# Kernel optimization log

Measured on AMD Instinct MI355X. Metric: run time of the kernel, lower is better.

## Reference

```python
import jax, jax.numpy as jnp
import numpy as np

N_CLASSES = 256
N_AUDIO_CHANS = 1
N_CHANS = 128
N_RES = 128
N_SKIP = 256
N_END = 256
KERNEL = 2
N_LAYERS = 10
N_STACKS = 3
DILATIONS = [2 ** i for _ in range(N_STACKS) for i in range(N_LAYERS)]
L = len(DILATIONS)
DN = ('NCW', 'OIW', 'NCW')


def setup_inputs() -> dict:
    key = jax.random.key(0)
    ks = jax.random.split(key, 16)
    s = 0.05  # small init keeps 30-layer residual stack numerically tame
    inp = {
        'x': jax.random.normal(ks[0], (4, N_AUDIO_CHANS, 16384), jnp.float32),
        'w_shift': jax.random.normal(ks[1], (N_CHANS, N_AUDIO_CHANS, KERNEL), jnp.float32) * s,
        'b_shift': jnp.zeros((N_CHANS,), jnp.float32),
        'conv_w': jax.random.normal(ks[2], (L, 2 * N_RES, N_CHANS, KERNEL), jnp.float32) * s,
        'conv_b': jnp.zeros((L, 2 * N_RES), jnp.float32),
        'res_w': jax.random.normal(ks[3], (L, N_CHANS, N_RES), jnp.float32) * s,
        'res_b': jnp.zeros((L, N_CHANS), jnp.float32),
        'skip_w': jax.random.normal(ks[4], (L, N_SKIP, N_RES), jnp.float32) * s,
        'skip_b': jnp.zeros((L, N_SKIP), jnp.float32),
        'a_w': jax.random.normal(ks[5], (N_END, N_SKIP), jnp.float32) * s,
        'a_b': jnp.zeros((N_END,), jnp.float32),
        'b_w': jax.random.normal(ks[6], (N_CLASSES * N_AUDIO_CHANS, N_END), jnp.float32) * s,
        'b_b': jnp.zeros((N_CLASSES * N_AUDIO_CHANS,), jnp.float32),
    }
    return inp


def _causal_conv(x, w, b, dilation):
    # left-pad by (k-1)*dilation so outputs depend only on past/present
    pad = (w.shape[-1] - 1) * dilation
    xp = jnp.pad(x, ((0, 0), (0, 0), (pad, 0)))
    y = jax.lax.conv_general_dilated(xp, w, window_strides=(1,), padding='VALID',
                                     rhs_dilation=(dilation,), dimension_numbers=DN)
    return y + b[None, :, None]


def reference(x, w_shift, b_shift, conv_w, conv_b, res_w, res_b,
              skip_w, skip_b, a_w, a_b, b_w, b_b):
    N, C, W = x.shape
    # shifted conv: shift input right by one (prepend 0, drop last), then causal conv
    xs = jnp.pad(x, ((0, 0), (0, 0), (1, 0)))[:, :, :-1]
    h = _causal_conv(xs, w_shift, b_shift, 1)  # (N, n_chans, W)

    skips = jnp.zeros((N, N_SKIP, W), h.dtype)
    for l in range(L):
        g = _causal_conv(h, conv_w[l], conv_b[l], DILATIONS[l])  # (N, 2*res, W)
        a, b_gate = jnp.split(g, 2, axis=1)
        gated = a * jax.nn.sigmoid(b_gate)                        # GLU, (N, res, W)
        h = jnp.einsum('or,nrw->now', res_w[l], gated) + res_b[l][None, :, None] + h
        skips = skips + jnp.einsum('or,nrw->now', skip_w[l], gated) + skip_b[l][None, :, None]

    z = jax.nn.relu(skips)
    z = jax.nn.relu(jnp.einsum('os,nsw->now', a_w, z) + a_b[None, :, None])
    logits = jnp.einsum('oe,new->now', b_w, z) + b_b[None, :, None]
    return logits.reshape(N, N_CLASSES, N_AUDIO_CHANS, W)
```

## Files before the change

### kernel.cpp

```cpp
#include <hip/hip_runtime.h>
#include <math.h>


#define NB 4
#define WLEN 16384
#define C 128
#define S 256
#define NLAYERS 30
#define TT 64
#define NTB (WLEN / TT)
#define XROW 264
#define GROW 136

#define SX(row, c) ((row) * 128 + ((c) ^ (((row) & 7) << 3)))

typedef _Float16 half8 __attribute__((ext_vector_type(8)));
typedef _Float16 half4 __attribute__((ext_vector_type(4)));
typedef float floatx4 __attribute__((ext_vector_type(4)));

__device__ __forceinline__ float sigmoidf_(float v) {
    return 1.0f / (1.0f + __expf(-v));
}

__global__ void prep_kernel(const float* __restrict__ conv_w,
                            const float* __restrict__ res_w,
                            const float* __restrict__ skip_w,
                            const float* __restrict__ a_w,
                            const float* __restrict__ b_w,
                            const float* __restrict__ conv_b,
                            const float* __restrict__ skip_b,
                            _Float16* __restrict__ cw,
                            _Float16* __restrict__ rsw,
                            _Float16* __restrict__ skw,
                            _Float16* __restrict__ aw,
                            _Float16* __restrict__ bw,
                            float* __restrict__ cbp,
                            float* __restrict__ ssum) {
    const int ncw = NLAYERS * 256 * 256;
    const int nrs = NLAYERS * 128 * 128;
    const int nsk = NLAYERS * 256 * 128;
    const int nab = 256 * 256;
    const int ncb = NLAYERS * 256;
    const int total = ncw + nrs + nsk + nab + nab + ncb + 256;
    for (int idx = blockIdx.x * blockDim.x + threadIdx.x; idx < total;
         idx += gridDim.x * blockDim.x) {
        int i = idx;
        if (i < ncw) {
            int j = i & 7, lane = (i >> 3) & 63, rest = i >> 9;
            int ks = rest & 7; rest >>= 3;
            int mt = rest & 15; int l = rest >> 4;
            int mp = mt * 16 + (lane & 15);
            int orow = (mp >> 1) + (mp & 1) * 128;
            int k = ks * 32 + (lane >> 4) * 8 + j;
            int tap = k >> 7, c = k & 127;
            cw[i] = (_Float16)conv_w[(((size_t)l * 256 + orow) * 128 + c) * 2 + tap];
        } else if (i < ncw + nrs) {
            i -= ncw;
            int j = i & 7, lane = (i >> 3) & 63, rest = i >> 9;
            int ks = rest & 3; rest >>= 2;
            int mt = rest & 7; int l = rest >> 3;
            int m = mt * 16 + (lane & 15);
            int k = ks * 32 + (lane >> 4) * 8 + j;
            rsw[i] = (_Float16)res_w[((size_t)l * 128 + m) * 128 + k];
        } else if (i < ncw + nrs + nsk) {
            i -= ncw + nrs;
            int j = i & 7, lane = (i >> 3) & 63, rest = i >> 9;
            int ks = rest & 3; rest >>= 2;
            int mt = rest & 15; int l = rest >> 4;
            int m = mt * 16 + (lane & 15);
            int k = ks * 32 + (lane >> 4) * 8 + j;
            skw[i] = (_Float16)skip_w[((size_t)l * 256 + m) * 128 + k];
        } else if (i < ncw + nrs + nsk + nab) {
            i -= ncw + nrs + nsk;
            int j = i & 7, lane = (i >> 3) & 63, rest = i >> 9;
            int ks = rest & 7; int mt = rest >> 3;
            aw[i] = (_Float16)a_w[(mt * 16 + (lane & 15)) * 256 + ks * 32 + (lane >> 4) * 8 + j];
        } else if (i < ncw + nrs + nsk + 2 * nab) {
            i -= ncw + nrs + nsk + nab;
            int j = i & 7, lane = (i >> 3) & 63, rest = i >> 9;
            int ks = rest & 7; int mt = rest >> 3;
            bw[i] = (_Float16)b_w[(mt * 16 + (lane & 15)) * 256 + ks * 32 + (lane >> 4) * 8 + j];
        } else if (i < ncw + nrs + nsk + 2 * nab + ncb) {
            i -= ncw + nrs + nsk + 2 * nab;
            int mp = i & 255; int l = i >> 8;
            cbp[i] = conv_b[l * 256 + (mp >> 1) + (mp & 1) * 128];
        } else {
            i -= ncw + nrs + nsk + 2 * nab + ncb;
            float s = 0.f;
            for (int l = 0; l < NLAYERS; ++l) s += skip_b[l * 256 + i];
            ssum[i] = s;
        }
    }
}

__global__ void front_kernel(const float* __restrict__ x,
                             const float* __restrict__ w_shift,
                             const float* __restrict__ b_shift,
                             _Float16* __restrict__ h) {
    const int n = blockIdx.y;
    const int t = blockIdx.x * 256 + threadIdx.x;
    float x1 = (t >= 1) ? x[n * WLEN + t - 1] : 0.0f;
    float x2 = (t >= 2) ? x[n * WLEN + t - 2] : 0.0f;
    _Float16* hq = h + ((size_t)n * WLEN + t) * 128;
    #pragma unroll
    for (int c0 = 0; c0 < 128; c0 += 8) {
        half8 v;
        #pragma unroll
        for (int j = 0; j < 8; ++j) {
            int c = c0 + j;
            v[j] = (_Float16)fmaf(w_shift[2 * c], x2,
                                  fmaf(w_shift[2 * c + 1], x1, b_shift[c]));
        }
        *(half8*)&hq[c0] = v;
    }
}

template <int E0, int NL, int NT, int HALO, bool FIRST>
__global__ __launch_bounds__(512)
__attribute__((amdgpu_waves_per_eu(2, 4))) void stack_kernel(
    const _Float16* __restrict__ h_in, _Float16* __restrict__ h_out,
    _Float16* __restrict__ chunk,
    const _Float16* __restrict__ cw0, const float* __restrict__ cb0,
    const _Float16* __restrict__ rsw0, const float* __restrict__ rb0,
    const _Float16* __restrict__ skw0, const float* __restrict__ ssum) {
    constexpr int WR = NT * 16;
    __shared__ _Float16 SMEM[2 * WR * 128];
    _Float16* H = SMEM;
    _Float16* G = SMEM + WR * 128;
    const int n = blockIdx.y, tb = blockIdx.x, t0 = tb * TT;
    const int tid = threadIdx.x;
    const int wave = __builtin_amdgcn_readfirstlane(tid >> 6);
    const int lane = tid & 63, q = lane >> 4, ml = lane & 15;

    floatx4 sacc[2][4];
    if (FIRST) {
        #pragma unroll
        for (int mt = 0; mt < 2; ++mt)
            #pragma unroll
            for (int r = 0; r < 4; ++r) {
                float bias = ssum[32 * wave + mt * 16 + q * 4 + r];
                #pragma unroll
                for (int nt = 0; nt < 4; ++nt) sacc[mt][nt][r] = bias;
            }
    } else {
        const _Float16* cp = chunk + ((size_t)n * NTB + tb) * 16384;
        #pragma unroll
        for (int mt = 0; mt < 2; ++mt)
            #pragma unroll
            for (int nt = 0; nt < 4; ++nt) {
                size_t o = (size_t)((((wave * 2 + mt) * 4) + nt) * 64 + lane) * 4;
                half4 v = *(const half4*)&cp[o];
                #pragma unroll
                for (int r = 0; r < 4; ++r) sacc[mt][nt][r] = (float)v[r];
            }
    }

    const _Float16* hn = h_in + (size_t)n * WLEN * 128;
    #pragma unroll
    for (int it = 0; it < (WR * 16 + 511) / 512; ++it) {
        int idx = it * 512 + tid;
        if (idx < WR * 16) {
            int seg = idx & 15;
            int w = idx >> 4;
            int src_t = t0 - HALO + w;
            half8 v = (half8)(_Float16)0.0f;
            if (src_t >= 0)
                v = *(const half8*)&hn[(size_t)src_t * 128 + seg * 8];
            *(half8*)&H[SX(w, seg * 8)] = v;
        }
    }
    __syncthreads();

    const _Float16* cw  = cw0;
    const float*    cb  = cb0;
    const _Float16* rsw = rsw0;
    const float*    rb  = rb0;
    const _Float16* skw = skw0;

    #pragma clang loop unroll(disable)
    for (int j = 0; j < NL; ++j) {
        const int d = 1 << (E0 + j);

        #pragma unroll
        for (int base = 0; base < NT; base += 4) {
            floatx4 acc[2][4];
            #pragma unroll
            for (int mt = 0; mt < 2; ++mt)
                #pragma unroll
                for (int r = 0; r < 4; ++r) {
                    float bias = cb[32 * wave + mt * 16 + q * 4 + r];
                    #pragma unroll
                    for (int nt = 0; nt < 4; ++nt) acc[mt][nt][r] = bias;
                }
            #pragma unroll
            for (int hp = 0; hp < 2; ++hp) {
                for (int ks = 0; ks < 4; ++ks) {
                    half8 a[2];
                    #pragma unroll
                    for (int mt = 0; mt < 2; ++mt)
                        a[mt] = *(const half8*)&cw[((((2 * wave + mt) * 8) + hp * 4 + ks) * 64 + lane) * 8];
                    #pragma unroll
                    for (int nt = 0; nt < 4; ++nt) {
                        if (base + nt < NT) {
                            int row = (base + nt) * 16 + ml;
                            if (!hp) { row -= d; if (row < 0) row = 0; }
                            half8 b = *(const half8*)&H[SX(row, ks * 32 + q * 8)];
                            #pragma unroll
                            for (int mt = 0; mt < 2; ++mt)
                                acc[mt][nt] = __builtin_amdgcn_mfma_f32_16x16x32_f16(a[mt], b, acc[mt][nt], 0, 0, 0);
                        }
                    }
                }
            }
            #pragma unroll
            for (int mt = 0; mt < 2; ++mt)
                #pragma unroll
                for (int nt = 0; nt < 4; ++nt) {
                    if (base + nt < NT) {
                        float g0 = acc[mt][nt][0] * sigmoidf_(acc[mt][nt][1]);
                        float g1 = acc[mt][nt][2] * sigmoidf_(acc[mt][nt][3]);
                        _Float16 p[2] = {(_Float16)g0, (_Float16)g1};
                        *(uint32_t*)&G[SX((base + nt) * 16 + ml, 16 * wave + mt * 8 + 2 * q)] = *(uint32_t*)p;
                    }
                }
        }
        __syncthreads();

        #pragma unroll
        for (int ks = 0; ks < 4; ++ks) {
            half8 a[2];
            #pragma unroll
            for (int mt = 0; mt < 2; ++mt)
                a[mt] = *(const half8*)&skw[((((2 * wave + mt) * 4) + ks) * 64 + lane) * 8];
            #pragma unroll
            for (int nt = 0; nt < 4; ++nt) {
                half8 b = *(const half8*)&G[SX(HALO + nt * 16 + ml, ks * 32 + q * 8)];
                #pragma unroll
                for (int mt = 0; mt < 2; ++mt)
                    sacc[mt][nt] = __builtin_amdgcn_mfma_f32_16x16x32_f16(a[mt], b, sacc[mt][nt], 0, 0, 0);
            }
        }

        #pragma unroll
        for (int base = 0; base < NT; base += 4) {
            floatx4 racc[4];
            #pragma unroll
            for (int r = 0; r < 4; ++r) {
                float bias = rb[16 * wave + q * 4 + r];
                #pragma unroll
                for (int nt = 0; nt < 4; ++nt) racc[nt][r] = bias;
            }
            #pragma unroll
            for (int ks = 0; ks < 4; ++ks) {
                half8 a = *(const half8*)&rsw[(((wave * 4) + ks) * 64 + lane) * 8];
                #pragma unroll
                for (int nt = 0; nt < 4; ++nt) {
                    if (base + nt < NT) {
                        half8 b = *(const half8*)&G[SX((base + nt) * 16 + ml, ks * 32 + q * 8)];
                        racc[nt] = __builtin_amdgcn_mfma_f32_16x16x32_f16(a, b, racc[nt], 0, 0, 0);
                    }
                }
            }
            #pragma unroll
            for (int nt = 0; nt < 4; ++nt) {
                if (base + nt < NT) {
                    int w = (base + nt) * 16 + ml;
                    int c = 16 * wave + q * 4;
                    half4 hv = *(const half4*)&H[SX(w, c)];
                    half4 o;
                    #pragma unroll
                    for (int r = 0; r < 4; ++r)
                        o[r] = (_Float16)(racc[nt][r] + (float)hv[r]);
                    *(half4*)&H[SX(w, c)] = o;
                }
            }
        }
        __syncthreads();

        cw  += 65536; cb += 256; rsw += 16384; rb += 128; skw += 32768;
    }

    _Float16* ho = h_out + (size_t)n * WLEN * 128;
    #pragma unroll
    for (int it = 0; it < 2; ++it) {
        int idx = it * 512 + tid;
        int seg = idx & 15;
        int w64 = idx >> 4;
        *(half8*)&ho[(size_t)(t0 + w64) * 128 + seg * 8] =
            *(const half8*)&H[SX(HALO + w64, seg * 8)];
    }

    {
        _Float16* cp = chunk + ((size_t)n * NTB + tb) * 16384;
        #pragma unroll
        for (int mt = 0; mt < 2; ++mt)
            #pragma unroll
            for (int nt = 0; nt < 4; ++nt) {
                size_t o = (size_t)((((wave * 2 + mt) * 4) + nt) * 64 + lane) * 4;
                half4 v;
                #pragma unroll
                for (int r = 0; r < 4; ++r) v[r] = (_Float16)sacc[mt][nt][r];
                *(half4*)&cp[o] = v;
            }
    }
}

__global__ __launch_bounds__(512, 8) void layer_kernel(
    const _Float16* __restrict__ h_in, _Float16* __restrict__ h_out,
    _Float16* __restrict__ chunk,
    const _Float16* __restrict__ cw, const float* __restrict__ cb,
    const _Float16* __restrict__ rsw, const float* __restrict__ rb,
    const _Float16* __restrict__ skw, int d) {
    __shared__ _Float16 SMEM[2 * TT * GROW];
    _Float16* X0 = SMEM;
    _Float16* X1 = SMEM + TT * GROW;
    _Float16* G  = X0;
    const int n = blockIdx.y, tb = blockIdx.x, t0 = tb * TT;
    const int tid = threadIdx.x;
    const int wave = __builtin_amdgcn_readfirstlane(tid >> 6);
    const int lane = tid & 63, q = lane >> 4, ml = lane & 15;

    const _Float16* hn = h_in + (size_t)n * WLEN * 128;
    #pragma unroll
    for (int it = 0; it < 4; ++it) {
        int idx = it * 512 + tid;
        int seg = idx & 15;
        int rowc = (idx >> 4) & 63;
        int tap = idx >> 10;
        int src_t = t0 + rowc - (tap ? 0 : d);
        half8 v = (half8)(_Float16)0.0f;
        if (src_t >= 0)
            v = *(const half8*)&hn[(size_t)src_t * 128 + seg * 8];
        _Float16* Xb = tap ? X1 : X0;
        *(half8*)&Xb[rowc * GROW + seg * 8] = v;
    }
    __syncthreads();

    floatx4 acc[2][4];
    #pragma unroll
    for (int mt = 0; mt < 2; ++mt)
        #pragma unroll
        for (int r = 0; r < 4; ++r) {
            float bias = cb[32 * wave + mt * 16 + q * 4 + r];
            #pragma unroll
            for (int nt = 0; nt < 4; ++nt) acc[mt][nt][r] = bias;
        }
    #pragma unroll
    for (int hp = 0; hp < 2; ++hp) {
        const _Float16* Xb = hp ? X1 : X0;
        for (int ks = 0; ks < 4; ++ks) {
            half8 a[2];
            #pragma unroll
            for (int mt = 0; mt < 2; ++mt)
                a[mt] = *(const half8*)&cw[((((2 * wave + mt) * 8) + hp * 4 + ks) * 64 + lane) * 8];
            #pragma unroll
            for (int nt = 0; nt < 4; ++nt) {
                half8 b = *(const half8*)&Xb[(nt * 16 + ml) * GROW + ks * 32 + q * 8];
                #pragma unroll
                for (int mt = 0; mt < 2; ++mt)
                    acc[mt][nt] = __builtin_amdgcn_mfma_f32_16x16x32_f16(a[mt], b, acc[mt][nt], 0, 0, 0);
            }
        }
    }
    __syncthreads();

    #pragma unroll
    for (int mt = 0; mt < 2; ++mt)
        #pragma unroll
        for (int nt = 0; nt < 4; ++nt) {
            float g0 = acc[mt][nt][0] * sigmoidf_(acc[mt][nt][1]);
            float g1 = acc[mt][nt][2] * sigmoidf_(acc[mt][nt][3]);
            _Float16 p[2] = {(_Float16)g0, (_Float16)g1};
            *(uint32_t*)&G[(nt * 16 + ml) * GROW + 16 * wave + mt * 8 + 2 * q] = *(uint32_t*)p;
        }
    __syncthreads();

    {
        floatx4 sacc[2][4];
        #pragma unroll
        for (int mt = 0; mt < 2; ++mt)
            #pragma unroll
            for (int nt = 0; nt < 4; ++nt)
                #pragma unroll
                for (int r = 0; r < 4; ++r) sacc[mt][nt][r] = 0.0f;
        #pragma unroll
        for (int ks = 0; ks < 4; ++ks) {
            half8 a[2];
            #pragma unroll
            for (int mt = 0; mt < 2; ++mt)
                a[mt] = *(const half8*)&skw[((((2 * wave + mt) * 4) + ks) * 64 + lane) * 8];
            #pragma unroll
            for (int nt = 0; nt < 4; ++nt) {
                half8 b = *(const half8*)&G[(nt * 16 + ml) * GROW + ks * 32 + q * 8];
                #pragma unroll
                for (int mt = 0; mt < 2; ++mt)
                    sacc[mt][nt] = __builtin_amdgcn_mfma_f32_16x16x32_f16(a[mt], b, sacc[mt][nt], 0, 0, 0);
            }
        }
        _Float16* cp = chunk + ((size_t)n * NTB + tb) * 16384;
        #pragma unroll
        for (int mt = 0; mt < 2; ++mt)
            #pragma unroll
            for (int nt = 0; nt < 4; ++nt) {
                size_t o = (size_t)((((wave * 2 + mt) * 4) + nt) * 64 + lane) * 4;
                half4 v = *(const half4*)&cp[o];
                half4 w;
                #pragma unroll
                for (int r = 0; r < 4; ++r)
                    w[r] = (_Float16)(sacc[mt][nt][r] + (float)v[r]);
                *(half4*)&cp[o] = w;
            }
    }

    {
        floatx4 racc[4];
        #pragma unroll
        for (int r = 0; r < 4; ++r) {
            float bias = rb[16 * wave + q * 4 + r];
            #pragma unroll
            for (int nt = 0; nt < 4; ++nt) racc[nt][r] = bias;
        }
        #pragma unroll
        for (int ks = 0; ks < 4; ++ks) {
            half8 a = *(const half8*)&rsw[(((wave * 4) + ks) * 64 + lane) * 8];
            #pragma unroll
            for (int nt = 0; nt < 4; ++nt) {
                half8 b = *(const half8*)&G[(nt * 16 + ml) * GROW + ks * 32 + q * 8];
                racc[nt] = __builtin_amdgcn_mfma_f32_16x16x32_f16(a, b, racc[nt], 0, 0, 0);
            }
        }
        _Float16* ho = h_out + (size_t)n * WLEN * 128;
        #pragma unroll
        for (int nt = 0; nt < 4; ++nt) {
            int tt = nt * 16 + ml;
            int c = 16 * wave + q * 4;
            half4 hv = *(const half4*)&X1[tt * GROW + c];
            half4 o;
            #pragma unroll
            for (int r = 0; r < 4; ++r)
                o[r] = (_Float16)(racc[nt][r] + (float)hv[r]);
            *(half4*)&ho[(size_t)(t0 + tt) * 128 + c] = o;
        }
    }
}

__global__ __launch_bounds__(512, 8) void last_head_kernel(
    const _Float16* __restrict__ h_in, const _Float16* __restrict__ chunk,
    float* __restrict__ out,
    const _Float16* __restrict__ cw, const float* __restrict__ cb,
    const _Float16* __restrict__ skw,
    const _Float16* __restrict__ aw, const float* __restrict__ ab,
    const _Float16* __restrict__ bw, const float* __restrict__ bb, int d) {
    __shared__ _Float16 SMEM[2 * TT * GROW];
    _Float16* X0 = SMEM;
    _Float16* X1 = SMEM + TT * GROW;
    _Float16* G  = X0;
    _Float16* X  = SMEM;
    const int n = blockIdx.y, tb = blockIdx.x, t0 = tb * TT;
    const int tid = threadIdx.x;
    const int wave = __builtin_amdgcn_readfirstlane(tid >> 6);
    const int lane = tid & 63, q = lane >> 4, ml = lane & 15;

    const _Float16* hn = h_in + (size_t)n * WLEN * 128;
    #pragma unroll
    for (int it = 0; it < 4; ++it) {
        int idx = it * 512 + tid;
        int seg = idx & 15;
        int rowc = (idx >> 4) & 63;
        int tap = idx >> 10;
        int src_t = t0 + rowc - (tap ? 0 : d);
        half8 v = (half8)(_Float16)0.0f;
        if (src_t >= 0)
            v = *(const half8*)&hn[(size_t)src_t * 128 + seg * 8];
        _Float16* Xb = tap ? X1 : X0;
        *(half8*)&Xb[rowc * GROW + seg * 8] = v;
    }
    __syncthreads();

    floatx4 acc[2][4];
    #pragma unroll
    for (int mt = 0; mt < 2; ++mt)
        #pragma unroll
        for (int r = 0; r < 4; ++r) {
            float bias = cb[32 * wave + mt * 16 + q * 4 + r];
            #pragma unroll
            for (int nt = 0; nt < 4; ++nt) acc[mt][nt][r] = bias;
        }
    #pragma unroll
    for (int hp = 0; hp < 2; ++hp) {
        const _Float16* Xb = hp ? X1 : X0;
        for (int ks = 0; ks < 4; ++ks) {
            half8 a[2];
            #pragma unroll
            for (int mt = 0; mt < 2; ++mt)
                a[mt] = *(const half8*)&cw[((((2 * wave + mt) * 8) + hp * 4 + ks) * 64 + lane) * 8];
            #pragma unroll
            for (int nt = 0; nt < 4; ++nt) {
                half8 b = *(const half8*)&Xb[(nt * 16 + ml) * GROW + ks * 32 + q * 8];
                #pragma unroll
                for (int mt = 0; mt < 2; ++mt)
                    acc[mt][nt] = __builtin_amdgcn_mfma_f32_16x16x32_f16(a[mt], b, acc[mt][nt], 0, 0, 0);
            }
        }
    }
    __syncthreads();

    #pragma unroll
    for (int mt = 0; mt < 2; ++mt)
        #pragma unroll
        for (int nt = 0; nt < 4; ++nt) {
            float g0 = acc[mt][nt][0] * sigmoidf_(acc[mt][nt][1]);
            float g1 = acc[mt][nt][2] * sigmoidf_(acc[mt][nt][3]);
            _Float16 p[2] = {(_Float16)g0, (_Float16)g1};
            *(uint32_t*)&G[(nt * 16 + ml) * GROW + 16 * wave + mt * 8 + 2 * q] = *(uint32_t*)p;
        }
    __syncthreads();

    half4 z[2][4];
    {
        floatx4 sacc[2][4];
        #pragma unroll
        for (int mt = 0; mt < 2; ++mt)
            #pragma unroll
            for (int nt = 0; nt < 4; ++nt)
                #pragma unroll
                for (int r = 0; r < 4; ++r) sacc[mt][nt][r] = 0.0f;
        #pragma unroll
        for (int ks = 0; ks < 4; ++ks) {
            half8 a[2];
            #pragma unroll
            for (int mt = 0; mt < 2; ++mt)
                a[mt] = *(const half8*)&skw[((((2 * wave + mt) * 4) + ks) * 64 + lane) * 8];
            #pragma unroll
            for (int nt = 0; nt < 4; ++nt) {
                half8 b = *(const half8*)&G[(nt * 16 + ml) * GROW + ks * 32 + q * 8];
                #pragma unroll
                for (int mt = 0; mt < 2; ++mt)
                    sacc[mt][nt] = __builtin_amdgcn_mfma_f32_16x16x32_f16(a[mt], b, sacc[mt][nt], 0, 0, 0);
            }
        }
        const _Float16* cp = chunk + ((size_t)n * NTB + tb) * 16384;
        #pragma unroll
        for (int mt = 0; mt < 2; ++mt)
            #pragma unroll
            for (int nt = 0; nt < 4; ++nt) {
                size_t o = (size_t)((((wave * 2 + mt) * 4) + nt) * 64 + lane) * 4;
                half4 v = *(const half4*)&cp[o];
                #pragma unroll
                for (int r = 0; r < 4; ++r) {
                    _Float16 s = (_Float16)(sacc[mt][nt][r] + (float)v[r]);
                    z[mt][nt][r] = (_Float16)fmaxf((float)s, 0.0f);
                }
            }
    }
    __syncthreads();

    #pragma unroll
    for (int mt = 0; mt < 2; ++mt)
        #pragma unroll
        for (int nt = 0; nt < 4; ++nt)
            *(half4*)&X[(nt * 16 + ml) * XROW + 32 * wave + mt * 16 + q * 4] = z[mt][nt];
    __syncthreads();

    #pragma unroll
    for (int mt = 0; mt < 2; ++mt)
        #pragma unroll
        for (int r = 0; r < 4; ++r) {
            float bias = ab[32 * wave + mt * 16 + q * 4 + r];
            #pragma unroll
            for (int nt = 0; nt < 4; ++nt) acc[mt][nt][r] = bias;
        }
    for (int ks = 0; ks < 8; ++ks) {
        half8 a[2];
        #pragma unroll
        for (int mt = 0; mt < 2; ++mt)
            a[mt] = *(const half8*)&aw[((((2 * wave + mt) * 8) + ks) * 64 + lane) * 8];
        #pragma unroll
        for (int nt = 0; nt < 4; ++nt) {
            half8 b = *(const half8*)&X[(nt * 16 + ml) * XROW + ks * 32 + q * 8];
            #pragma unroll
            for (int mt = 0; mt < 2; ++mt)
                acc[mt][nt] = __builtin_amdgcn_mfma_f32_16x16x32_f16(a[mt], b, acc[mt][nt], 0, 0, 0);
        }
    }
    __syncthreads();
    #pragma unroll
    for (int mt = 0; mt < 2; ++mt)
        #pragma unroll
        for (int nt = 0; nt < 4; ++nt) {
            half4 zz;
            #pragma unroll
            for (int r = 0; r < 4; ++r)
                zz[r] = (_Float16)fmaxf(acc[mt][nt][r], 0.0f);
            *(half4*)&X[(nt * 16 + ml) * XROW + 32 * wave + mt * 16 + q * 4] = zz;
        }
    __syncthreads();

    #pragma unroll
    for (int mt = 0; mt < 2; ++mt)
        #pragma unroll
        for (int r = 0; r < 4; ++r) {
            float bias = bb[32 * wave + mt * 16 + q * 4 + r];
            #pragma unroll
            for (int nt = 0; nt < 4; ++nt) acc[mt][nt][r] = bias;
        }
    for (int ks = 0; ks < 8; ++ks) {
        half8 a[2];
        #pragma unroll
        for (int mt = 0; mt < 2; ++mt)
            a[mt] = *(const half8*)&bw[((((2 * wave + mt) * 8) + ks) * 64 + lane) * 8];
        #pragma unroll
        for (int nt = 0; nt < 4; ++nt) {
            half8 b = *(const half8*)&X[(nt * 16 + ml) * XROW + ks * 32 + q * 8];
            #pragma unroll
            for (int mt = 0; mt < 2; ++mt)
                acc[mt][nt] = __builtin_amdgcn_mfma_f32_16x16x32_f16(a[mt], b, acc[mt][nt], 0, 0, 0);
        }
    }
    float* on = out + (size_t)n * S * WLEN;
    #pragma unroll
    for (int mt = 0; mt < 2; ++mt)
        #pragma unroll
        for (int nt = 0; nt < 4; ++nt)
            #pragma unroll
            for (int r = 0; r < 4; ++r) {
                int o = 32 * wave + mt * 16 + q * 4 + r;
                int tt = t0 + nt * 16 + ml;
                on[(size_t)o * WLEN + tt] = acc[mt][nt][r];
            }
}

extern "C" void kernel_launch(void* const* d_in, const int* in_sizes, int n_in,
                              void* d_out, int out_size, void* d_ws, size_t ws_size,
                              hipStream_t stream) {
    (void)in_sizes; (void)n_in; (void)out_size; (void)ws_size;
    const float* x       = (const float*)d_in[0];
    const float* w_shift = (const float*)d_in[1];
    const float* b_shift = (const float*)d_in[2];
    const float* conv_w  = (const float*)d_in[3];
    const float* conv_b  = (const float*)d_in[4];
    const float* res_w   = (const float*)d_in[5];
    const float* res_b   = (const float*)d_in[6];
    const float* skip_w  = (const float*)d_in[7];
    const float* skip_b  = (const float*)d_in[8];
    const float* a_w     = (const float*)d_in[9];
    const float* a_b     = (const float*)d_in[10];
    const float* b_w     = (const float*)d_in[11];
    const float* b_b     = (const float*)d_in[12];
    float* out = (float*)d_out;

    char* ws = (char*)d_ws;
    size_t off = 0;
    _Float16* hA    = (_Float16*)(ws + off); off += (size_t)NB * WLEN * 128 * 2;
    _Float16* hB    = (_Float16*)(ws + off); off += (size_t)NB * WLEN * 128 * 2;
    _Float16* chunk = (_Float16*)(ws + off); off += (size_t)NB * NTB * 16384 * 2;
    _Float16* cw  = (_Float16*)(ws + off); off += (size_t)NLAYERS * 256 * 256 * 2;
    _Float16* rsw = (_Float16*)(ws + off); off += (size_t)NLAYERS * 128 * 128 * 2;
    _Float16* skw = (_Float16*)(ws + off); off += (size_t)NLAYERS * 256 * 128 * 2;
    _Float16* aw  = (_Float16*)(ws + off); off += 256 * 256 * 2;
    _Float16* bw  = (_Float16*)(ws + off); off += 256 * 256 * 2;
    float* cbp  = (float*)(ws + off); off += (size_t)NLAYERS * 256 * 4;
    float* ssum = (float*)(ws + off); off += 256 * 4;

    prep_kernel<<<512, 256, 0, stream>>>(conv_w, res_w, skip_w, a_w, b_w,
                                         conv_b, skip_b,
                                         cw, rsw, skw, aw, bw, cbp, ssum);
    front_kernel<<<dim3(WLEN / 256, NB), 256, 0, stream>>>(x, w_shift, b_shift, hA);

    const dim3 grid(NTB, NB);
    _Float16* hin = hA;
    _Float16* hout = hB;
    for (int s = 0; s < 3; ++s) {
        const int l0 = s * 10;
        if (s == 0)
            stack_kernel<0, 4, 5, 16, true><<<grid, 512, 0, stream>>>(
                hin, hout, chunk,
                cw + (size_t)l0 * 65536, cbp + l0 * 256,
                rsw + (size_t)l0 * 16384, res_b + l0 * 128,
                skw + (size_t)l0 * 32768, ssum);
        else
            stack_kernel<0, 4, 5, 16, false><<<grid, 512, 0, stream>>>(
                hin, hout, chunk,
                cw + (size_t)l0 * 65536, cbp + l0 * 256,
                rsw + (size_t)l0 * 16384, res_b + l0 * 128,
                skw + (size_t)l0 * 32768, ssum);
        { _Float16* tmp = hin; hin = hout; hout = tmp; }
        for (int jj = 4; jj < 10; ++jj) {
            const int l = l0 + jj;
            const int dil = 1 << jj;
            if (l == NLAYERS - 1) {
                last_head_kernel<<<grid, 512, 0, stream>>>(
                    hin, chunk, out,
                    cw + (size_t)l * 65536, cbp + l * 256,
                    skw + (size_t)l * 32768,
                    aw, a_b, bw, b_b, dil);
            } else {
                layer_kernel<<<grid, 512, 0, stream>>>(
                    hin, hout, chunk,
                    cw + (size_t)l * 65536, cbp + l * 256,
                    rsw + (size_t)l * 16384, res_b + l * 128,
                    skw + (size_t)l * 32768, dil);
                _Float16* tmp = hin; hin = hout; hout = tmp;
            }
        }
    }
}
```

Baseline: 1.026 ms.

## Zero-pad activation buffers and load layer inputs directly into LDS

Activation buffers get a zeroed left-padding region of 512 time rows per batch, so causal loads no longer need bounds checks. The layer kernels now fetch input tiles with global_load_lds, writing straight to shared memory without passing through registers. Shared-memory tiles switch from padded rows to the XOR-swizzled layout to avoid bank conflicts, and the global source address is pre-swizzled to match. This adds an extra pad kernel launch and a larger workspace, and relies on the direct-to-LDS load writing in wave-contiguous order.

```diff
diff --git a/kernel.cpp b/kernel.cpp
--- a/kernel.cpp
+++ b/kernel.cpp
@@ -10,7 +10,8 @@
 #define TT 64
 #define NTB (WLEN / TT)
 #define XROW 264
-#define GROW 136
+#define PAD 512
+#define HROWS (WLEN + PAD)
 
 #define SX(row, c) ((row) * 128 + ((c) ^ (((row) & 7) << 3)))
 
@@ -93,6 +94,18 @@
     }
 }
 
+__global__ void pad_kernel(_Float16* __restrict__ hA, _Float16* __restrict__ hB) {
+    const size_t tot = (size_t)NB * PAD * 16;
+    size_t i = (size_t)blockIdx.x * blockDim.x + threadIdx.x;
+    if (i < 2 * tot) {
+        _Float16* h = (i < tot) ? hA : hB;
+        size_t j = (i < tot) ? i : i - tot;
+        size_t nn = j / (PAD * 16);
+        size_t k = j % (PAD * 16);
+        *(half8*)&h[nn * (size_t)HROWS * 128 + k * 8] = (half8)(_Float16)0.0f;
+    }
+}
+
 __global__ void front_kernel(const float* __restrict__ x,
                              const float* __restrict__ w_shift,
                              const float* __restrict__ b_shift,
@@ -101,7 +114,7 @@
     const int t = blockIdx.x * 256 + threadIdx.x;
     float x1 = (t >= 1) ? x[n * WLEN + t - 1] : 0.0f;
     float x2 = (t >= 2) ? x[n * WLEN + t - 2] : 0.0f;
-    _Float16* hq = h + ((size_t)n * WLEN + t) * 128;
+    _Float16* hq = h + ((size_t)n * HROWS + PAD + t) * 128;
     #pragma unroll
     for (int c0 = 0; c0 < 128; c0 += 8) {
         half8 v;
@@ -155,7 +168,7 @@
             }
     }
 
-    const _Float16* hn = h_in + (size_t)n * WLEN * 128;
+    const _Float16* hn = h_in + ((size_t)n * HROWS + PAD) * 128;
     #pragma unroll
     for (int it = 0; it < (WR * 16 + 511) / 512; ++it) {
         int idx = it * 512 + tid;
@@ -163,9 +176,7 @@
             int seg = idx & 15;
             int w = idx >> 4;
             int src_t = t0 - HALO + w;
-            half8 v = (half8)(_Float16)0.0f;
-            if (src_t >= 0)
-                v = *(const half8*)&hn[(size_t)src_t * 128 + seg * 8];
+            half8 v = *(const half8*)&hn[(size_t)src_t * 128 + seg * 8];
             *(half8*)&H[SX(w, seg * 8)] = v;
         }
     }
@@ -280,7 +291,7 @@
         cw  += 65536; cb += 256; rsw += 16384; rb += 128; skw += 32768;
     }
 
-    _Float16* ho = h_out + (size_t)n * WLEN * 128;
+    _Float16* ho = h_out + ((size_t)n * HROWS + PAD) * 128;
     #pragma unroll
     for (int it = 0; it < 2; ++it) {
         int idx = it * 512 + tid;
@@ -311,28 +322,30 @@
     const _Float16* __restrict__ cw, const float* __restrict__ cb,
     const _Float16* __restrict__ rsw, const float* __restrict__ rb,
     const _Float16* __restrict__ skw, int d) {
-    __shared__ _Float16 SMEM[2 * TT * GROW];
+    __shared__ _Float16 SMEM[2 * TT * 128];
     _Float16* X0 = SMEM;
-    _Float16* X1 = SMEM + TT * GROW;
+    _Float16* X1 = SMEM + TT * 128;
     _Float16* G  = X0;
     const int n = blockIdx.y, tb = blockIdx.x, t0 = tb * TT;
     const int tid = threadIdx.x;
     const int wave = __builtin_amdgcn_readfirstlane(tid >> 6);
     const int lane = tid & 63, q = lane >> 4, ml = lane & 15;
 
-    const _Float16* hn = h_in + (size_t)n * WLEN * 128;
+    const _Float16* hn = h_in + ((size_t)n * HROWS + PAD) * 128;
     #pragma unroll
     for (int it = 0; it < 4; ++it) {
-        int idx = it * 512 + tid;
-        int seg = idx & 15;
-        int rowc = (idx >> 4) & 63;
-        int tap = idx >> 10;
+        int idxw = it * 512 + (wave << 6);
+        int lidx = idxw + lane;
+        int seg  = lidx & 15;
+        int rowc = (lidx >> 4) & 63;
+        int tap  = lidx >> 10;
         int src_t = t0 + rowc - (tap ? 0 : d);
-        half8 v = (half8)(_Float16)0.0f;
-        if (src_t >= 0)
-            v = *(const half8*)&hn[(size_t)src_t * 128 + seg * 8];
-        _Float16* Xb = tap ? X1 : X0;
-        *(half8*)&Xb[rowc * GROW + seg * 8] = v;
+        int segs = seg ^ (rowc & 7);
+        const _Float16* g = &hn[(size_t)src_t * 128 + segs * 8];
+        _Float16* lb = SMEM + (size_t)idxw * 8;
+        __builtin_amdgcn_global_load_lds(
+            (const __attribute__((address_space(1))) void*)g,
+            (__attribute__((address_space(3))) void*)lb, 16, 0, 0);
     }
     __syncthreads();
 
@@ -355,7 +368,7 @@
                 a[mt] = *(const half8*)&cw[((((2 * wave + mt) * 8) + hp * 4 + ks) * 64 + lane) * 8];
             #pragma unroll
             for (int nt = 0; nt < 4; ++nt) {
-                half8 b = *(const half8*)&Xb[(nt * 16 + ml) * GROW + ks * 32 + q * 8];
+                half8 b = *(const half8*)&Xb[SX(nt * 16 + ml, ks * 32 + q * 8)];
                 #pragma unroll
                 for (int mt = 0; mt < 2; ++mt)
                     acc[mt][nt] = __builtin_amdgcn_mfma_f32_16x16x32_f16(a[mt], b, acc[mt][nt], 0, 0, 0);
@@ -371,7 +384,7 @@
             float g0 = acc[mt][nt][0] * sigmoidf_(acc[mt][nt][1]);
             float g1 = acc[mt][nt][2] * sigmoidf_(acc[mt][nt][3]);
             _Float16 p[2] = {(_Float16)g0, (_Float16)g1};
-            *(uint32_t*)&G[(nt * 16 + ml) * GROW + 16 * wave + mt * 8 + 2 * q] = *(uint32_t*)p;
+            *(uint32_t*)&G[SX(nt * 16 + ml, 16 * wave + mt * 8 + 2 * q)] = *(uint32_t*)p;
         }
     __syncthreads();
 
@@ -391,7 +404,7 @@
                 a[mt] = *(const half8*)&skw[((((2 * wave + mt) * 4) + ks) * 64 + lane) * 8];
             #pragma unroll
             for (int nt = 0; nt < 4; ++nt) {
-                half8 b = *(const half8*)&G[(nt * 16 + ml) * GROW + ks * 32 + q * 8];
+                half8 b = *(const half8*)&G[SX(nt * 16 + ml, ks * 32 + q * 8)];
                 #pragma unroll
                 for (int mt = 0; mt < 2; ++mt)
                     sacc[mt][nt] = __builtin_amdgcn_mfma_f32_16x16x32_f16(a[mt], b, sacc[mt][nt], 0, 0, 0);
@@ -425,16 +438,16 @@
             half8 a = *(const half8*)&rsw[(((wave * 4) + ks) * 64 + lane) * 8];
             #pragma unroll
             for (int nt = 0; nt < 4; ++nt) {
-                half8 b = *(const half8*)&G[(nt * 16 + ml) * GROW + ks * 32 + q * 8];
+                half8 b = *(const half8*)&G[SX(nt * 16 + ml, ks * 32 + q * 8)];
                 racc[nt] = __builtin_amdgcn_mfma_f32_16x16x32_f16(a, b, racc[nt], 0, 0, 0);
             }
         }
-        _Float16* ho = h_out + (size_t)n * WLEN * 128;
+        _Float16* ho = h_out + ((size_t)n * HROWS + PAD) * 128;
         #pragma unroll
         for (int nt = 0; nt < 4; ++nt) {
             int tt = nt * 16 + ml;
             int c = 16 * wave + q * 4;
-            half4 hv = *(const half4*)&X1[tt * GROW + c];
+            half4 hv = *(const half4*)&X1[SX(tt, c)];
             half4 o;
             #pragma unroll
             for (int r = 0; r < 4; ++r)
@@ -451,9 +464,9 @@
     const _Float16* __restrict__ skw,
     const _Float16* __restrict__ aw, const float* __restrict__ ab,
     const _Float16* __restrict__ bw, const float* __restrict__ bb, int d) {
-    __shared__ _Float16 SMEM[2 * TT * GROW];
+    __shared__ _Float16 SMEM[TT * XROW];
     _Float16* X0 = SMEM;
-    _Float16* X1 = SMEM + TT * GROW;
+    _Float16* X1 = SMEM + TT * 128;
     _Float16* G  = X0;
     _Float16* X  = SMEM;
     const int n = blockIdx.y, tb = blockIdx.x, t0 = tb * TT;
@@ -461,19 +474,21 @@
     const int wave = __builtin_amdgcn_readfirstlane(tid >> 6);
     const int lane = tid & 63, q = lane >> 4, ml = lane & 15;
 
-    const _Float16* hn = h_in + (size_t)n * WLEN * 128;
+    const _Float16* hn = h_in + ((size_t)n * HROWS + PAD) * 128;
     #pragma unroll
     for (int it = 0; it < 4; ++it) {
-        int idx = it * 512 + tid;
-        int seg = idx & 15;
-        int rowc = (idx >> 4) & 63;
-        int tap = idx >> 10;
+        int idxw = it * 512 + (wave << 6);
+        int lidx = idxw + lane;
+        int seg  = lidx & 15;
+        int rowc = (lidx >> 4) & 63;
+        int tap  = lidx >> 10;
         int src_t = t0 + rowc - (tap ? 0 : d);
-        half8 v = (half8)(_Float16)0.0f;
-        if (src_t >= 0)
-            v = *(const half8*)&hn[(size_t)src_t * 128 + seg * 8];
-        _Float16* Xb = tap ? X1 : X0;
-        *(half8*)&Xb[rowc * GROW + seg * 8] = v;
+        int segs = seg ^ (rowc & 7);
+        const _Float16* g = &hn[(size_t)src_t * 128 + segs * 8];
+        _Float16* lb = SMEM + (size_t)idxw * 8;
+        __builtin_amdgcn_global_load_lds(
+            (const __attribute__((address_space(1))) void*)g,
+            (__attribute__((address_space(3))) void*)lb, 16, 0, 0);
     }
     __syncthreads();
 
@@ -496,7 +511,7 @@
                 a[mt] = *(const half8*)&cw[((((2 * wave + mt) * 8) + hp * 4 + ks) * 64 + lane) * 8];
             #pragma unroll
             for (int nt = 0; nt < 4; ++nt) {
-                half8 b = *(const half8*)&Xb[(nt * 16 + ml) * GROW + ks * 32 + q * 8];
+                half8 b = *(const half8*)&Xb[SX(nt * 16 + ml, ks * 32 + q * 8)];
                 #pragma unroll
                 for (int mt = 0; mt < 2; ++mt)
                     acc[mt][nt] = __builtin_amdgcn_mfma_f32_16x16x32_f16(a[mt], b, acc[mt][nt], 0, 0, 0);
@@ -512,7 +527,7 @@
             float g0 = acc[mt][nt][0] * sigmoidf_(acc[mt][nt][1]);
             float g1 = acc[mt][nt][2] * sigmoidf_(acc[mt][nt][3]);
             _Float16 p[2] = {(_Float16)g0, (_Float16)g1};
-            *(uint32_t*)&G[(nt * 16 + ml) * GROW + 16 * wave + mt * 8 + 2 * q] = *(uint32_t*)p;
+            *(uint32_t*)&G[SX(nt * 16 + ml, 16 * wave + mt * 8 + 2 * q)] = *(uint32_t*)p;
         }
     __syncthreads();
 
@@ -533,7 +548,7 @@
                 a[mt] = *(const half8*)&skw[((((2 * wave + mt) * 4) + ks) * 64 + lane) * 8];
             #pragma unroll
             for (int nt = 0; nt < 4; ++nt) {
-                half8 b = *(const half8*)&G[(nt * 16 + ml) * GROW + ks * 32 + q * 8];
+                half8 b = *(const half8*)&G[SX(nt * 16 + ml, ks * 32 + q * 8)];
                 #pragma unroll
                 for (int mt = 0; mt < 2; ++mt)
                     sacc[mt][nt] = __builtin_amdgcn_mfma_f32_16x16x32_f16(a[mt], b, sacc[mt][nt], 0, 0, 0);
@@ -651,8 +666,8 @@
 
     char* ws = (char*)d_ws;
     size_t off = 0;
-    _Float16* hA    = (_Float16*)(ws + off); off += (size_t)NB * WLEN * 128 * 2;
-    _Float16* hB    = (_Float16*)(ws + off); off += (size_t)NB * WLEN * 128 * 2;
+    _Float16* hA    = (_Float16*)(ws + off); off += (size_t)NB * HROWS * 128 * 2;
+    _Float16* hB    = (_Float16*)(ws + off); off += (size_t)NB * HROWS * 128 * 2;
     _Float16* chunk = (_Float16*)(ws + off); off += (size_t)NB * NTB * 16384 * 2;
     _Float16* cw  = (_Float16*)(ws + off); off += (size_t)NLAYERS * 256 * 256 * 2;
     _Float16* rsw = (_Float16*)(ws + off); off += (size_t)NLAYERS * 128 * 128 * 2;
@@ -665,6 +680,7 @@
     prep_kernel<<<512, 256, 0, stream>>>(conv_w, res_w, skip_w, a_w, b_w,
                                          conv_b, skip_b,
                                          cw, rsw, skw, aw, bw, cbp, ssum);
+    pad_kernel<<<256, 256, 0, stream>>>(hA, hB);
     front_kernel<<<dim3(WLEN / 256, NB), 256, 0, stream>>>(x, w_shift, b_shift, hA);
 
     const dim3 grid(NTB, NB);
```

After: 1.054 ms. 1.03x slower.
